# Kernel tuning notes

Measured on AMD Instinct MI355X. Metric: run time of the kernel, lower is better.

## Reference

```python
import jax, jax.numpy as jnp
import numpy as np

B, N, F = 16, 1024, 256
HEADS, K, DOUT = 8, 512, 256
TAU = 1.0
EPS = 1e-08


def setup_inputs() -> dict:
    key = jax.random.key(0)
    k1, k2, k3, k4, k5, k6 = jax.random.split(key, 6)
    return {
        'Q': jax.random.normal(k1, (B, N, F), dtype=jnp.float32),
        'keys': jax.random.uniform(k2, (HEADS, K, F), dtype=jnp.float32),
        'conv_w': jax.random.normal(k3, (HEADS,), dtype=jnp.float32),
        'lin_w': jax.random.normal(k4, (DOUT, F), dtype=jnp.float32) * 0.05,
        'lin_b': jax.random.normal(k5, (DOUT,), dtype=jnp.float32) * 0.05,
        'mask': jax.random.randint(k6, (B, N), 0, 2, dtype=jnp.int32),
    }


def kl_reg(C):
    # C: (B, N, K)
    P = C ** 2
    cn = jnp.sum(C, axis=-2, keepdims=True) + EPS          # sum over N
    P = P / cn
    pn = jnp.sum(P, axis=-1, keepdims=True) + EPS          # sum over K
    P = P / pn
    kl = jnp.sum(P * (jnp.log(P + EPS) - jnp.log(C + EPS)))
    return 100.0 * kl


def memconv_fwd(Q, keys, conv_w, lin_w, lin_b, fmask):
    # pairwise L2 distance Q (B,N,F) vs keys (H,K,F) -> C (B,H,N,K)
    q2 = jnp.sum(Q * Q, axis=-1)                            # (B,N)
    k2 = jnp.sum(keys * keys, axis=-1)                      # (H,K)
    qk = jnp.einsum('bnf,hkf->bhnk', Q, keys)               # (B,H,N,K)
    d2 = q2[:, None, :, None] + k2[None, :, None, :] - 2.0 * qk
    C = jnp.sqrt(jnp.maximum(d2, 0.0))
    em = fmask[:, None, :, None]                            # (B,1,N,1) broadcast
    C = C * em
    # student-t kernel (gmn variant)
    C = (1.0 + C ** 2 / TAU) ** (-(0.5 * TAU + 0.5))
    C = C / jnp.sum(C, axis=-1, keepdims=True)
    C = C * em
    # conv1x1 over heads -> (B,N,K)
    C = jnp.einsum('bhnk,h->bnk', C, conv_w)
    C = jax.nn.softmax(C, axis=-1)
    C = C * fmask[:, :, None]
    kl = kl_reg(C)
    V = jnp.einsum('bnk,bnf->bkf', C, Q)                    # (B,K,F)
    out = jax.nn.leaky_relu(jnp.einsum('bkf,of->bko', V, lin_w) + lin_b, 0.01)
    return out, kl


def reference(Q, keys, conv_w, lin_w, lin_b, mask):
    fmask = mask.astype(Q.dtype)
    return memconv_fwd(Q, keys, conv_w, lin_w, lin_b, fmask)
```

## Files before the change

### kernel.cpp

```cpp
#include <hip/hip_runtime.h>
#include <math.h>

#define Bc 16
#define Nc 1024
#define Fc 256
#define Hc 8
#define Kc 512
#define DOUTc 256
#define EPSc 1e-8f

typedef short v8s __attribute__((ext_vector_type(8)));
typedef float v4f __attribute__((ext_vector_type(4)));

__device__ __forceinline__ float waveReduceSum(float v) {
    v += __shfl_xor(v, 32); v += __shfl_xor(v, 16); v += __shfl_xor(v, 8);
    v += __shfl_xor(v, 4);  v += __shfl_xor(v, 2);  v += __shfl_xor(v, 1);
    return v;
}

__device__ __forceinline__ unsigned short f2bf(float f) {
    unsigned int u = __float_as_uint(f);
    u = (u + 0x7fffu + ((u >> 16) & 1u)) >> 16;
    return (unsigned short)u;
}

__device__ __forceinline__ void lds_barrier() {
    __builtin_amdgcn_s_waitcnt(0xC07F);
    __builtin_amdgcn_s_barrier();
}

__global__ __launch_bounds__(256) void prep_all(
    const float* __restrict__ Q, const float* __restrict__ keys,
    const float* __restrict__ lin_w,
    float* __restrict__ k2g, unsigned short* __restrict__ Kp,
    unsigned short* __restrict__ Qbp, unsigned short* __restrict__ Wp,
    float* __restrict__ cn, float* __restrict__ klout) {
    __shared__ unsigned short T2[32][66];
    const int bx = blockIdx.x;
    const int tid = threadIdx.x;
    if (bx < 1024) {
        int row = bx * 4 + (tid >> 6);
        int l = tid & 63;
        float4 v = *(const float4*)(keys + (size_t)row * Fc + l * 4);
        float s = v.x * v.x + v.y * v.y + v.z * v.z + v.w * v.w;
        s = waveReduceSum(s);
        if (l == 0) k2g[row] = s;
    } else if (bx < 1536) {
        int t = (bx - 1024) * 256 + tid;
        int lane = t & 63, ci = t >> 6;
        int ct = ci & 7, ks = (ci >> 3) & 7, wv = (ci >> 6) & 3, h = ci >> 8;
        int qd = lane >> 4, li = lane & 15;
        int col = h * 512 + wv * 128 + ct * 16 + li;
        const float* src = keys + (size_t)col * Fc + ks * 32 + qd * 8;
        float4 a = *(const float4*)src;
        float4 b = *(const float4*)(src + 4);
        *(ushort4*)(Kp + (size_t)t * 8) = make_ushort4(f2bf(a.x), f2bf(a.y), f2bf(a.z), f2bf(a.w));
        *(ushort4*)(Kp + (size_t)t * 8 + 4) = make_ushort4(f2bf(b.x), f2bf(b.y), f2bf(b.z), f2bf(b.w));
    } else if (bx < 3584) {
        int i = bx - 1536;
        int n0 = (i & 31) * 32, f0 = ((i >> 5) & 3) * 64, bb = i >> 7;
        {
            int n_l = tid >> 3, f_l = (tid & 7) * 8;
            const float* src = Q + ((size_t)(bb * Nc + n0 + n_l)) * Fc + f0 + f_l;
            float4 a = *(const float4*)src;
            float4 b = *(const float4*)(src + 4);
            T2[n_l][f_l + 0] = f2bf(a.x); T2[n_l][f_l + 1] = f2bf(a.y);
            T2[n_l][f_l + 2] = f2bf(a.z); T2[n_l][f_l + 3] = f2bf(a.w);
            T2[n_l][f_l + 4] = f2bf(b.x); T2[n_l][f_l + 5] = f2bf(b.y);
            T2[n_l][f_l + 6] = f2bf(b.z); T2[n_l][f_l + 7] = f2bf(b.w);
        }
        __syncthreads();
        int c = tid >> 6, L = tid & 63;
        int qd = L >> 4, li = L & 15;
        unsigned short o[8];
#pragma unroll
        for (int j = 0; j < 8; j++) o[j] = T2[qd * 8 + j][c * 16 + li];
        size_t idx = ((((size_t)bb * 16 + (f0 >> 4) + c) * 32 + (n0 >> 5)) * 64 + L) * 8;
        *(ushort4*)(Qbp + idx) = make_ushort4(o[0], o[1], o[2], o[3]);
        *(ushort4*)(Qbp + idx + 4) = make_ushort4(o[4], o[5], o[6], o[7]);
    } else if (bx < 3616) {
        int t = (bx - 3584) * 256 + tid;
        int lane = t & 63, ci = t >> 6;
        int ot = ci >> 3, fs = ci & 7;
        int qd = lane >> 4, li = lane & 15;
        const float* src = lin_w + (size_t)(ot * 16 + li) * Fc + fs * 32 + qd * 8;
        float4 a = *(const float4*)src;
        float4 b = *(const float4*)(src + 4);
        *(ushort4*)(Wp + (size_t)t * 8) = make_ushort4(f2bf(a.x), f2bf(a.y), f2bf(a.z), f2bf(a.w));
        *(ushort4*)(Wp + (size_t)t * 8 + 4) = make_ushort4(f2bf(b.x), f2bf(b.y), f2bf(b.z), f2bf(b.w));
    } else {
        int i = (bx - 3616) * 256 + tid;
        float4 z = make_float4(0.f, 0.f, 0.f, 0.f);
        float4* d = (float4*)(cn + (size_t)i * 16);
        d[0] = z; d[1] = z; d[2] = z; d[3] = z;
        if (bx == 3616 && tid == 0) *klout = 0.f;
    }
}

__global__ __launch_bounds__(256, 1) void cmfma_kernel(
    const float* __restrict__ Q, const unsigned short* __restrict__ Kp,
    const float* __restrict__ k2g, const float* __restrict__ conv_w,
    const int* __restrict__ mask, float* __restrict__ C,
    float* __restrict__ cn, unsigned short* __restrict__ Ctp) {
    __shared__ float k2s[Hc * Kc];
    __shared__ float q2s[32];
    __shared__ float msh[32];
    __shared__ float redb[Hc][4][32];
    __shared__ float mslot[4][32];
    __shared__ float eslot[4][32];
    __shared__ short Tb[512][36];
    const int tid = threadIdx.x;
    const int wv = tid >> 6, L = tid & 63;
    const int qd = L >> 4, li = L & 15;
    const int gr0 = blockIdx.x * 32;
    const int b = gr0 >> 10;

    v8s A[2][8];
    {
        float q2part[2] = {0.f, 0.f};
#pragma unroll
        for (int s = 0; s < 2; s++) {
            const float* qrow = Q + (size_t)(gr0 + s * 16 + li) * Fc + qd * 8;
#pragma unroll
            for (int ks = 0; ks < 8; ks++) {
                float4 a = *(const float4*)(qrow + ks * 32);
                float4 bq = *(const float4*)(qrow + ks * 32 + 4);
                v8s f;
                f[0] = (short)f2bf(a.x);  f[1] = (short)f2bf(a.y);
                f[2] = (short)f2bf(a.z);  f[3] = (short)f2bf(a.w);
                f[4] = (short)f2bf(bq.x); f[5] = (short)f2bf(bq.y);
                f[6] = (short)f2bf(bq.z); f[7] = (short)f2bf(bq.w);
                A[s][ks] = f;
                q2part[s] += a.x * a.x + a.y * a.y + a.z * a.z + a.w * a.w +
                             bq.x * bq.x + bq.y * bq.y + bq.z * bq.z + bq.w * bq.w;
            }
            q2part[s] += __shfl_xor(q2part[s], 16);
            q2part[s] += __shfl_xor(q2part[s], 32);
            if (qd == 0 && wv == 0) q2s[s * 16 + li] = q2part[s];
        }
    }
    if (tid < 32) msh[tid] = (float)mask[gr0 + tid];
    for (int i = tid; i < Hc * Kc / 4; i += 256)
        *(float4*)&k2s[i * 4] = *(const float4*)(k2g + i * 4);

    v4f D[2][8], S[2][8];
#pragma unroll
    for (int s = 0; s < 2; s++)
#pragma unroll
        for (int ct = 0; ct < 8; ct++) {
            D[s][ct] = (v4f){0.f, 0.f, 0.f, 0.f};
            S[s][ct] = (v4f){0.f, 0.f, 0.f, 0.f};
        }

    const unsigned short* kwbase = Kp + (size_t)L * 8;
    v8s Bc0[8], Bn[8];
    {
        const unsigned short* p0 = kwbase + (size_t)(wv * 64) * 512;
#pragma unroll
        for (int ct = 0; ct < 8; ct++) Bc0[ct] = *(const v8s*)(p0 + ct * 512);
    }

    lds_barrier();

    float q2r[2][4], mrow[2][4];
#pragma unroll
    for (int s = 0; s < 2; s++)
#pragma unroll
        for (int r = 0; r < 4; r++) {
            q2r[s][r] = q2s[s * 16 + qd * 4 + r];
            mrow[s][r] = msh[s * 16 + qd * 4 + r];
        }

#define KSTEP(kk, CUR, NXT)                                                        \
    do {                                                                           \
        int hn = h * 8 + (kk) + 1;                                                 \
        int hh = (hn >> 3) & 7, kn = hn & 7;                                       \
        const unsigned short* pb =                                                 \
            kwbase + (size_t)(((hh * 4 + wv) * 64 + kn * 8)) * 512;                \
        _Pragma("unroll") for (int ct = 0; ct < 8; ct++)                           \
            NXT[ct] = *(const v8s*)(pb + ct * 512);                                \
        _Pragma("unroll") for (int ct = 0; ct < 8; ct++)                           \
            D[0][ct] = __builtin_amdgcn_mfma_f32_16x16x32_bf16(A[0][kk], CUR[ct],  \
                                                               D[0][ct], 0, 0, 0);\
        _Pragma("unroll") for (int ct = 0; ct < 8; ct++)                           \
            D[1][ct] = __builtin_amdgcn_mfma_f32_16x16x32_bf16(A[1][kk], CUR[ct],  \
                                                               D[1][ct], 0, 0, 0);\
    } while (0)

    for (int h = 0; h < Hc; ++h) {
        KSTEP(0, Bc0, Bn); KSTEP(1, Bn, Bc0);
        KSTEP(2, Bc0, Bn); KSTEP(3, Bn, Bc0);
        KSTEP(4, Bc0, Bn); KSTEP(5, Bn, Bc0);
        KSTEP(6, Bc0, Bn); KSTEP(7, Bn, Bc0);

        float rs[2][4] = {{0.f, 0.f, 0.f, 0.f}, {0.f, 0.f, 0.f, 0.f}};
#pragma unroll
        for (int ct = 0; ct < 8; ct++) {
            float k2v = k2s[h * Kc + wv * 128 + ct * 16 + li];
#pragma unroll
            for (int s = 0; s < 2; s++)
#pragma unroll
                for (int r = 0; r < 4; r++) {
                    float d2 = fmaxf(q2r[s][r] + k2v - 2.f * D[s][ct][r], 0.f) * mrow[s][r];
                    float t = __builtin_amdgcn_rcpf(1.f + d2);
                    D[s][ct][r] = t;
                    rs[s][r] += t;
                }
        }
#pragma unroll
        for (int s = 0; s < 2; s++)
#pragma unroll
            for (int r = 0; r < 4; r++) {
                rs[s][r] += __shfl_xor(rs[s][r], 1, 16);
                rs[s][r] += __shfl_xor(rs[s][r], 2, 16);
                rs[s][r] += __shfl_xor(rs[s][r], 4, 16);
                rs[s][r] += __shfl_xor(rs[s][r], 8, 16);
            }
        if (li == 0) {
#pragma unroll
            for (int s = 0; s < 2; s++)
#pragma unroll
                for (int r = 0; r < 4; r++) redb[h][wv][s * 16 + qd * 4 + r] = rs[s][r];
        }
        lds_barrier();
        float wh = conv_w[h];
        float sc[2][4];
#pragma unroll
        for (int s = 0; s < 2; s++)
#pragma unroll
            for (int r = 0; r < 4; r++) {
                int rw = s * 16 + qd * 4 + r;
                float tot = redb[h][0][rw] + redb[h][1][rw] + redb[h][2][rw] + redb[h][3][rw];
                sc[s][r] = wh * __builtin_amdgcn_rcpf(tot);
            }
#pragma unroll
        for (int s = 0; s < 2; s++)
#pragma unroll
            for (int ct = 0; ct < 8; ct++)
#pragma unroll
                for (int r = 0; r < 4; r++) {
                    S[s][ct][r] += sc[s][r] * D[s][ct][r];
                    D[s][ct][r] = 0.f;
                }
    }
#undef KSTEP

    float mx[2][4] = {{-1e30f, -1e30f, -1e30f, -1e30f}, {-1e30f, -1e30f, -1e30f, -1e30f}};
#pragma unroll
    for (int s = 0; s < 2; s++)
#pragma unroll
        for (int ct = 0; ct < 8; ct++)
#pragma unroll
            for (int r = 0; r < 4; r++) mx[s][r] = fmaxf(mx[s][r], S[s][ct][r]);
#pragma unroll
    for (int s = 0; s < 2; s++)
#pragma unroll
        for (int r = 0; r < 4; r++) {
            mx[s][r] = fmaxf(mx[s][r], __shfl_xor(mx[s][r], 1, 16));
            mx[s][r] = fmaxf(mx[s][r], __shfl_xor(mx[s][r], 2, 16));
            mx[s][r] = fmaxf(mx[s][r], __shfl_xor(mx[s][r], 4, 16));
            mx[s][r] = fmaxf(mx[s][r], __shfl_xor(mx[s][r], 8, 16));
        }
    if (li == 0) {
#pragma unroll
        for (int s = 0; s < 2; s++)
#pragma unroll
            for (int r = 0; r < 4; r++) mslot[wv][s * 16 + qd * 4 + r] = mx[s][r];
    }
    lds_barrier();
#pragma unroll
    for (int s = 0; s < 2; s++)
#pragma unroll
        for (int r = 0; r < 4; r++) {
            int rw = s * 16 + qd * 4 + r;
            mx[s][r] = fmaxf(fmaxf(mslot[0][rw], mslot[1][rw]),
                             fmaxf(mslot[2][rw], mslot[3][rw]));
        }
    float es[2][4] = {{0.f, 0.f, 0.f, 0.f}, {0.f, 0.f, 0.f, 0.f}};
#pragma unroll
    for (int s = 0; s < 2; s++)
#pragma unroll
        for (int ct = 0; ct < 8; ct++)
#pragma unroll
            for (int r = 0; r < 4; r++) {
                float e = __expf(S[s][ct][r] - mx[s][r]);
                S[s][ct][r] = e;
                es[s][r] += e;
            }
#pragma unroll
    for (int s = 0; s < 2; s++)
#pragma unroll
        for (int r = 0; r < 4; r++) {
            es[s][r] += __shfl_xor(es[s][r], 1, 16);
            es[s][r] += __shfl_xor(es[s][r], 2, 16);
            es[s][r] += __shfl_xor(es[s][r], 4, 16);
            es[s][r] += __shfl_xor(es[s][r], 8, 16);
        }
    if (li == 0) {
#pragma unroll
        for (int s = 0; s < 2; s++)
#pragma unroll
            for (int r = 0; r < 4; r++) eslot[wv][s * 16 + qd * 4 + r] = es[s][r];
    }
    lds_barrier();
    float inv[2][4];
#pragma unroll
    for (int s = 0; s < 2; s++)
#pragma unroll
        for (int r = 0; r < 4; r++) {
            int rw = s * 16 + qd * 4 + r;
            float tot = eslot[0][rw] + eslot[1][rw] + eslot[2][rw] + eslot[3][rw];
            inv[s][r] = mrow[s][r] / tot;
        }
#pragma unroll
    for (int ct = 0; ct < 8; ct++) {
        int k = wv * 128 + ct * 16 + li;
        float colsum = 0.f;
#pragma unroll
        for (int s = 0; s < 2; s++) {
            float cv[4];
#pragma unroll
            for (int r = 0; r < 4; r++) {
                cv[r] = S[s][ct][r] * inv[s][r];
                C[(size_t)(gr0 + s * 16 + qd * 4 + r) * Kc + k] = cv[r];
                colsum += cv[r];
            }
            short4 t4;
            t4.x = (short)f2bf(cv[0]); t4.y = (short)f2bf(cv[1]);
            t4.z = (short)f2bf(cv[2]); t4.w = (short)f2bf(cv[3]);
            *(short4*)&Tb[k][s * 16 + qd * 4] = t4;
        }
        colsum += __shfl_xor(colsum, 16);
        colsum += __shfl_xor(colsum, 32);
        if (qd == 0) atomicAdd(&cn[b * Kc + k], colsum);
    }
    lds_barrier();
    {
        const int ns0 = (gr0 & 1023) >> 5;
#pragma unroll
        for (int kk = 0; kk < 2; kk++) {
            int k = tid * 2 + kk;
            int kt = k >> 4, klo = k & 15;
            size_t cbase = (((size_t)b * 32 + kt) * 32 + ns0) * 512;
#pragma unroll
            for (int q2i = 0; q2i < 4; q2i++) {
                short4 lo = *(short4*)&Tb[k][q2i * 8];
                short4 hi = *(short4*)&Tb[k][q2i * 8 + 4];
                short4* d = (short4*)(Ctp + cbase + (size_t)(q2i * 16 + klo) * 8);
                d[0] = lo; d[1] = hi;
            }
        }
    }
}

__global__ __launch_bounds__(256) void klv_kernel(
    const unsigned short* __restrict__ Ctp, const unsigned short* __restrict__ Qbp,
    unsigned short* __restrict__ Vp, const float* __restrict__ C,
    const float* __restrict__ cn, float* __restrict__ klout) {
    __shared__ short Vt[64][76];
    __shared__ float red[4];
    int tid = threadIdx.x;
    int bx = blockIdx.x;
    if (bx < 512) {
        int w = tid >> 6, L = tid & 63;
        int qd = L >> 4, li = L & 15;
        int wr = w >> 1, wc = w & 1;
        int bb = bx >> 5;
        int rem = bx & 31;
        int ktb = rem >> 2, ftb = rem & 3;
        int KT0 = ktb * 4 + wr * 2;
        int FT0 = ftb * 4 + wc * 2;
        const unsigned short* pa0 = Ctp + (((size_t)bb * 32 + KT0) * 32) * 512 + L * 8;
        const unsigned short* pa1 = pa0 + (size_t)32 * 512;
        const unsigned short* pb0 = Qbp + (((size_t)bb * 16 + FT0) * 32) * 512 + L * 8;
        const unsigned short* pb1 = pb0 + (size_t)32 * 512;
        v4f acc[2][2];
#pragma unroll
        for (int a = 0; a < 2; a++)
#pragma unroll
            for (int c = 0; c < 2; c++) acc[a][c] = (v4f){0.f, 0.f, 0.f, 0.f};

        v8s A0 = *(const v8s*)pa0, A1 = *(const v8s*)pa1;
        v8s B0 = *(const v8s*)pb0, B1 = *(const v8s*)pb1;
        for (int ns = 0; ns < 32; ns++) {
            int nsn = (ns + 1) & 31;
            v8s A0n = *(const v8s*)(pa0 + nsn * 512);
            v8s A1n = *(const v8s*)(pa1 + nsn * 512);
            v8s B0n = *(const v8s*)(pb0 + nsn * 512);
            v8s B1n = *(const v8s*)(pb1 + nsn * 512);
            acc[0][0] = __builtin_amdgcn_mfma_f32_16x16x32_bf16(A0, B0, acc[0][0], 0, 0, 0);
            acc[0][1] = __builtin_amdgcn_mfma_f32_16x16x32_bf16(A0, B1, acc[0][1], 0, 0, 0);
            acc[1][0] = __builtin_amdgcn_mfma_f32_16x16x32_bf16(A1, B0, acc[1][0], 0, 0, 0);
            acc[1][1] = __builtin_amdgcn_mfma_f32_16x16x32_bf16(A1, B1, acc[1][1], 0, 0, 0);
            A0 = A0n; A1 = A1n; B0 = B0n; B1 = B1n;
        }
#pragma unroll
        for (int a = 0; a < 2; a++)
#pragma unroll
            for (int c = 0; c < 2; c++)
#pragma unroll
                for (int r = 0; r < 4; r++)
                    Vt[(wr * 2 + a) * 16 + qd * 4 + r][(wc * 2 + c) * 16 + li] =
                        (short)f2bf(acc[a][c][r]);
        __syncthreads();
        {
            int ci = tid >> 5, s5 = tid & 31;
            int mtl = ci >> 1, fsl = ci & 1;
            size_t mt_g = (size_t)bb * 32 + ktb * 4 + mtl;
            size_t fs_g = (size_t)ftb * 2 + fsl;
#pragma unroll
            for (int half = 0; half < 2; half++) {
                int L2 = s5 + half * 32;
                int qd2 = L2 >> 4, li2 = L2 & 15;
                short4 x0 = *(short4*)&Vt[mtl * 16 + li2][fsl * 32 + qd2 * 8];
                short4 x1 = *(short4*)&Vt[mtl * 16 + li2][fsl * 32 + qd2 * 8 + 4];
                short4* d = (short4*)(Vp + ((mt_g * 8 + fs_g) * 64 + L2) * 8);
                d[0] = x0; d[1] = x1;
            }
        }
    } else {
        int bk = bx - 512;
        int w = tid >> 6, l = tid & 63;
        float kacc = 0.f;
#pragma unroll
        for (int rr = 0; rr < 4; rr++) {
            int row = bk * 16 + w * 4 + rr;
            int b = row >> 10;
            const float* cp = C + (size_t)row * Kc + l * 8;
            const float* np = cn + b * Kc + l * 8;
            float4 c0 = *(const float4*)cp;
            float4 c1 = *(const float4*)(cp + 4);
            float4 n0 = *(const float4*)np;
            float4 n1 = *(const float4*)(np + 4);
            float p[8];
            p[0] = c0.x * c0.x / (n0.x + EPSc); p[1] = c0.y * c0.y / (n0.y + EPSc);
            p[2] = c0.z * c0.z / (n0.z + EPSc); p[3] = c0.w * c0.w / (n0.w + EPSc);
            p[4] = c1.x * c1.x / (n1.x + EPSc); p[5] = c1.y * c1.y / (n1.y + EPSc);
            p[6] = c1.z * c1.z / (n1.z + EPSc); p[7] = c1.w * c1.w / (n1.w + EPSc);
            float s = p[0] + p[1] + p[2] + p[3] + p[4] + p[5] + p[6] + p[7];
            float pn = waveReduceSum(s) + EPSc;
            float rpn = 1.0f / pn;
            float cc[8] = {c0.x, c0.y, c0.z, c0.w, c1.x, c1.y, c1.z, c1.w};
#pragma unroll
            for (int j = 0; j < 8; j++) {
                float P = p[j] * rpn;
                kacc += P * __logf((P + EPSc) / (cc[j] + EPSc));
            }
        }
        kacc = waveReduceSum(kacc);
        if (l == 0) red[w] = kacc;
        __syncthreads();
        if (tid == 0)
            atomicAdd(klout, 100.f * (red[0] + red[1] + red[2] + red[3]));
    }
}

__global__ __launch_bounds__(256) void ofma_kernel(
    const unsigned short* __restrict__ Vp, const unsigned short* __restrict__ Wp,
    const float* __restrict__ bias, float* __restrict__ out) {
    int tid = threadIdx.x;
    int w = tid >> 6, L = tid & 63;
    int qd = L >> 4, li = L & 15;
    int wr = w >> 1, wc = w & 1;
    int MT0 = blockIdx.x * 4 + wr * 2;
    int OT0 = blockIdx.y * 4 + wc * 2;
    const unsigned short* pa0 = Vp + ((size_t)MT0 * 8) * 512 + L * 8;
    const unsigned short* pa1 = pa0 + (size_t)8 * 512;
    const unsigned short* pb0 = Wp + ((size_t)OT0 * 8) * 512 + L * 8;
    const unsigned short* pb1 = pb0 + (size_t)8 * 512;
    v4f acc[2][2];
#pragma unroll
    for (int a = 0; a < 2; a++)
#pragma unroll
        for (int c = 0; c < 2; c++) acc[a][c] = (v4f){0.f, 0.f, 0.f, 0.f};
#pragma unroll
    for (int fs = 0; fs < 8; fs++) {
        v8s A0 = *(const v8s*)(pa0 + fs * 512);
        v8s A1 = *(const v8s*)(pa1 + fs * 512);
        v8s B0 = *(const v8s*)(pb0 + fs * 512);
        v8s B1 = *(const v8s*)(pb1 + fs * 512);
        acc[0][0] = __builtin_amdgcn_mfma_f32_16x16x32_bf16(A0, B0, acc[0][0], 0, 0, 0);
        acc[0][1] = __builtin_amdgcn_mfma_f32_16x16x32_bf16(A0, B1, acc[0][1], 0, 0, 0);
        acc[1][0] = __builtin_amdgcn_mfma_f32_16x16x32_bf16(A1, B0, acc[1][0], 0, 0, 0);
        acc[1][1] = __builtin_amdgcn_mfma_f32_16x16x32_bf16(A1, B1, acc[1][1], 0, 0, 0);
    }
#pragma unroll
    for (int c = 0; c < 2; c++) {
        float bv = bias[(OT0 + c) * 16 + li];
#pragma unroll
        for (int a = 0; a < 2; a++)
#pragma unroll
            for (int r = 0; r < 4; r++) {
                int m = (MT0 + a) * 16 + qd * 4 + r;
                int o = (OT0 + c) * 16 + li;
                float x = acc[a][c][r] + bv;
                out[(size_t)m * DOUTc + o] = x > 0.f ? x : 0.01f * x;
            }
    }
}

extern "C" void kernel_launch(void* const* d_in, const int* in_sizes, int n_in,
                              void* d_out, int out_size, void* d_ws, size_t ws_size,
                              hipStream_t stream) {
    const float* Q = (const float*)d_in[0];
    const float* keys = (const float*)d_in[1];
    const float* conv_w = (const float*)d_in[2];
    const float* lin_w = (const float*)d_in[3];
    const float* lin_b = (const float*)d_in[4];
    const int* mask = (const int*)d_in[5];

    float* out = (float*)d_out;
    float* kl = out + (size_t)Bc * Kc * DOUTc;

    float* ws = (float*)d_ws;
    float* C = ws;
    float* k2 = C + (size_t)Bc * Nc * Kc;
    float* cn = k2 + (size_t)Hc * Kc;
    unsigned short* Kp = (unsigned short*)(cn + (size_t)Bc * Kc);
    unsigned short* Ctp = Kp + (size_t)Hc * Kc * Fc;
    unsigned short* Qbp = Ctp + (size_t)Bc * Nc * Kc;
    unsigned short* Vp = Qbp + (size_t)Bc * Nc * Fc;
    unsigned short* Wp = Vp + (size_t)Bc * Kc * Fc;

    prep_all<<<3618, 256, 0, stream>>>(Q, keys, lin_w, k2, Kp, Qbp, Wp, cn, kl);
    cmfma_kernel<<<Bc * Nc / 32, 256, 0, stream>>>(Q, Kp, k2, conv_w, mask, C, cn, Ctp);
    klv_kernel<<<1536, 256, 0, stream>>>(Ctp, Qbp, Vp, C, cn, kl);
    ofma_kernel<<<dim3(Bc * Kc / 64, DOUTc / 64), 256, 0, stream>>>(Vp, Wp, lin_b, out);
}
```

Measured before the change: 192.8 us.

## Stage bf16 Q fragments in LDS and alias shared buffers to fit two blocks per CU

The Q A-fragments are no longer held in 64 VGPRs for the whole kernel. They are written once to LDS and reloaded one k-step ahead inside the MFMA loop. Shared memory is unioned so k2s and Ash share space with the transpose buffer Tb, and launch bounds are raised to 2 blocks per CU. The Q load and bf16 conversion is also split across all four waves instead of being repeated per wave. The aim is higher occupancy to hide global K-fragment load latency, at the cost of extra LDS reads in the inner loop and possible register spilling under the tighter bound.

```diff
diff --git a/kernel.cpp b/kernel.cpp
--- a/kernel.cpp
+++ b/kernel.cpp
@@ -97,47 +97,49 @@
     }
 }
 
-__global__ __launch_bounds__(256, 1) void cmfma_kernel(
+__global__ __launch_bounds__(256, 2) void cmfma_kernel(
     const float* __restrict__ Q, const unsigned short* __restrict__ Kp,
     const float* __restrict__ k2g, const float* __restrict__ conv_w,
     const int* __restrict__ mask, float* __restrict__ C,
     float* __restrict__ cn, unsigned short* __restrict__ Ctp) {
-    __shared__ float k2s[Hc * Kc];
-    __shared__ float q2s[32];
+    __shared__ __align__(16) char uni[36864];
+    __shared__ float q2h[4][16];
     __shared__ float msh[32];
     __shared__ float redb[Hc][4][32];
     __shared__ float mslot[4][32];
     __shared__ float eslot[4][32];
-    __shared__ short Tb[512][36];
+    float* k2s = (float*)uni;
+    short* Ash = (short*)(uni + 16384);
+    short (*Tb)[36] = (short (*)[36])uni;
+
     const int tid = threadIdx.x;
     const int wv = tid >> 6, L = tid & 63;
     const int qd = L >> 4, li = L & 15;
     const int gr0 = blockIdx.x * 32;
     const int b = gr0 >> 10;
 
-    v8s A[2][8];
     {
-        float q2part[2] = {0.f, 0.f};
-#pragma unroll
-        for (int s = 0; s < 2; s++) {
-            const float* qrow = Q + (size_t)(gr0 + s * 16 + li) * Fc + qd * 8;
-#pragma unroll
-            for (int ks = 0; ks < 8; ks++) {
-                float4 a = *(const float4*)(qrow + ks * 32);
-                float4 bq = *(const float4*)(qrow + ks * 32 + 4);
-                v8s f;
-                f[0] = (short)f2bf(a.x);  f[1] = (short)f2bf(a.y);
-                f[2] = (short)f2bf(a.z);  f[3] = (short)f2bf(a.w);
-                f[4] = (short)f2bf(bq.x); f[5] = (short)f2bf(bq.y);
-                f[6] = (short)f2bf(bq.z); f[7] = (short)f2bf(bq.w);
-                A[s][ks] = f;
-                q2part[s] += a.x * a.x + a.y * a.y + a.z * a.z + a.w * a.w +
-                             bq.x * bq.x + bq.y * bq.y + bq.z * bq.z + bq.w * bq.w;
-            }
-            q2part[s] += __shfl_xor(q2part[s], 16);
-            q2part[s] += __shfl_xor(q2part[s], 32);
-            if (qd == 0 && wv == 0) q2s[s * 16 + li] = q2part[s];
-        }
+        int s_ = wv >> 1;
+        int ksbase = (wv & 1) * 4;
+        const float* qrow = Q + (size_t)(gr0 + s_ * 16 + li) * Fc + qd * 8;
+        float q2part = 0.f;
+#pragma unroll
+        for (int j = 0; j < 4; j++) {
+            int ks = ksbase + j;
+            float4 a = *(const float4*)(qrow + ks * 32);
+            float4 bq = *(const float4*)(qrow + ks * 32 + 4);
+            v8s f;
+            f[0] = (short)f2bf(a.x);  f[1] = (short)f2bf(a.y);
+            f[2] = (short)f2bf(a.z);  f[3] = (short)f2bf(a.w);
+            f[4] = (short)f2bf(bq.x); f[5] = (short)f2bf(bq.y);
+            f[6] = (short)f2bf(bq.z); f[7] = (short)f2bf(bq.w);
+            *(v8s*)&Ash[(((s_ * 8 + ks) * 64) + L) * 8] = f;
+            q2part += a.x * a.x + a.y * a.y + a.z * a.z + a.w * a.w +
+                      bq.x * bq.x + bq.y * bq.y + bq.z * bq.z + bq.w * bq.w;
+        }
+        q2part += __shfl_xor(q2part, 16);
+        q2part += __shfl_xor(q2part, 32);
+        if (qd == 0) q2h[wv][li] = q2part;
     }
     if (tid < 32) msh[tid] = (float)mask[gr0 + tid];
     for (int i = tid; i < Hc * Kc / 4; i += 256)
@@ -167,9 +169,14 @@
     for (int s = 0; s < 2; s++)
 #pragma unroll
         for (int r = 0; r < 4; r++) {
-            q2r[s][r] = q2s[s * 16 + qd * 4 + r];
+            q2r[s][r] = q2h[2 * s][qd * 4 + r] + q2h[2 * s + 1][qd * 4 + r];
             mrow[s][r] = msh[s * 16 + qd * 4 + r];
         }
+
+#define LD_A(s, kk) (*(const v8s*)&Ash[(((s) * 8 + (kk)) * 64 + L) * 8])
+
+    v8s Ac0 = LD_A(0, 0);
+    v8s Ac1 = LD_A(1, 0);
 
 #define KSTEP(kk, CUR, NXT)                                                        \
     do {                                                                           \
@@ -179,12 +186,15 @@
             kwbase + (size_t)(((hh * 4 + wv) * 64 + kn * 8)) * 512;                \
         _Pragma("unroll") for (int ct = 0; ct < 8; ct++)                           \
             NXT[ct] = *(const v8s*)(pb + ct * 512);                                \
+        v8s An0 = LD_A(0, ((kk) + 1) & 7);                                         \
+        v8s An1 = LD_A(1, ((kk) + 1) & 7);                                         \
         _Pragma("unroll") for (int ct = 0; ct < 8; ct++)                           \
-            D[0][ct] = __builtin_amdgcn_mfma_f32_16x16x32_bf16(A[0][kk], CUR[ct],  \
+            D[0][ct] = __builtin_amdgcn_mfma_f32_16x16x32_bf16(Ac0, CUR[ct],       \
                                                                D[0][ct], 0, 0, 0);\
         _Pragma("unroll") for (int ct = 0; ct < 8; ct++)                           \
-            D[1][ct] = __builtin_amdgcn_mfma_f32_16x16x32_bf16(A[1][kk], CUR[ct],  \
+            D[1][ct] = __builtin_amdgcn_mfma_f32_16x16x32_bf16(Ac1, CUR[ct],       \
                                                                D[1][ct], 0, 0, 0);\
+        Ac0 = An0; Ac1 = An1;                                                      \
     } while (0)
 
     for (int h = 0; h < Hc; ++h) {
@@ -244,6 +254,7 @@
                 }
     }
 #undef KSTEP
+#undef LD_A
 
     float mx[2][4] = {{-1e30f, -1e30f, -1e30f, -1e30f}, {-1e30f, -1e30f, -1e30f, -1e30f}};
 #pragma unroll
```

Result: faster. 165.7 us (-14.1%).
